# Kernel optimization log

Hardware: AMD Instinct MI355X
Metric: run time of the kernel (lower is better)

## Reference

```python
import jax, jax.numpy as jnp
import numpy as np

B = 2048
F = 267          # frame_size
L = 32           # latent_size
H = 256          # hidden_size (hard-coded in module)
E = 8            # num_experts
G = 64           # gate hidden size (hard-coded)
IN0 = L + F      # decoder layer0 input (latent + frame*cond_frames)
IN1 = L + H      # decoder inter input
OUT = F          # num_future_predictions * frame_size


def _lin_init(key, out_dim, in_dim):
    # kaiming-uniform-like scale
    bound = float(np.sqrt(1.0 / in_dim))
    return jax.random.uniform(key, (out_dim, in_dim), jnp.float32, -bound, bound)


def setup_inputs() -> dict:
    key = jax.random.key(0)
    ks = jax.random.split(key, 24)
    d = {}
    d["x"] = jax.random.normal(ks[0], (B, F), jnp.float32)
    d["c"] = jax.random.normal(ks[1], (B, F), jnp.float32)
    # encoder
    d["fc1_w"] = _lin_init(ks[2], H, 2 * F); d["fc1_b"] = jnp.zeros((H,), jnp.float32)
    d["fc2_w"] = _lin_init(ks[3], H, F + H); d["fc2_b"] = jnp.zeros((H,), jnp.float32)
    d["mu_w"] = _lin_init(ks[4], L, F + H);  d["mu_b"] = jnp.zeros((L,), jnp.float32)
    d["lv_w"] = _lin_init(ks[5], L, F + H);  d["lv_b"] = jnp.zeros((L,), jnp.float32)
    # gate
    d["g0_w"] = _lin_init(ks[6], G, IN0); d["g0_b"] = jnp.zeros((G,), jnp.float32)
    d["g1_w"] = _lin_init(ks[7], G, G);   d["g1_b"] = jnp.zeros((G,), jnp.float32)
    d["g2_w"] = _lin_init(ks[8], E, G);   d["g2_b"] = jnp.zeros((E,), jnp.float32)
    # expert weights [E, in, out], biases [E, out], bias filled 0.01 as in module
    d["w0"] = jax.random.uniform(ks[9], (E, IN0, H), jnp.float32, -1, 1) * np.sqrt(1.0 / IN0)
    d["b0"] = jnp.full((E, H), 0.01, jnp.float32)
    d["w1"] = jax.random.uniform(ks[10], (E, IN1, H), jnp.float32, -1, 1) * np.sqrt(1.0 / IN1)
    d["b1"] = jnp.full((E, H), 0.01, jnp.float32)
    d["w2"] = jax.random.uniform(ks[11], (E, IN1, OUT), jnp.float32, -1, 1) * np.sqrt(1.0 / IN1)
    d["b2"] = jnp.full((E, OUT), 0.01, jnp.float32)
    return d


def reference(x, c, fc1_w, fc1_b, fc2_w, fc2_b, mu_w, mu_b, lv_w, lv_b,
              g0_w, g0_b, g1_w, g1_b, g2_w, g2_b, w0, b0, w1, b1, w2, b2):
    elu = jax.nn.elu
    # ---- encoder ----
    h1 = elu(jnp.concatenate([x, c], axis=1) @ fc1_w.T + fc1_b)
    h2 = elu(jnp.concatenate([x, h1], axis=1) @ fc2_w.T + fc2_b)
    s = jnp.concatenate([x, h2], axis=1)
    mu = s @ mu_w.T + mu_b
    logvar = s @ lv_w.T + lv_b
    eps = jax.random.normal(jax.random.key(42), mu.shape, mu.dtype)
    z = mu + eps * jnp.exp(0.5 * logvar)
    # ---- mixed decoder ----
    g = elu(jnp.concatenate([z, c], axis=1) @ g0_w.T + g0_b)
    g = elu(g @ g1_w.T + g1_b)
    coeff = jax.nn.softmax(g @ g2_w.T + g2_b, axis=1)  # [B, E]
    layer_out = c
    for (W, bvec, act) in ((w0, b0, True), (w1, b1, True), (w2, b2, False)):
        inp = jnp.concatenate([z, layer_out], axis=1)          # [B, in]
        # per-expert GEMM then coefficient mixing (same math as per-sample
        # mixed-weight bmm: coeff @ flat_weight then baddbmm)
        out = jnp.einsum('be,bi,eio->bo', coeff, inp, W, optimize=True)
        out = out + coeff @ bvec                               # mixed bias
        layer_out = elu(out) if act else out
    return (layer_out, mu, logvar)
```

## Files before the change

### kernel.cpp

```cpp
#include <hip/hip_runtime.h>
#include <math.h>
#include <stdint.h>

#define DI __device__ __forceinline__

typedef __attribute__((ext_vector_type(8))) short bf16x8;
typedef __attribute__((ext_vector_type(4))) float f32x4;
typedef __attribute__((ext_vector_type(4))) int i32x4;

DI float elu_f(float v) { return v > 0.f ? v : expm1f(v); }

DI unsigned short f2bf(float f) {
  uint32_t u = __float_as_uint(f);
  return (unsigned short)((u + 0x7FFFu + ((u >> 16) & 1u)) >> 16);
}

DI void threefry2x32(uint32_t k0, uint32_t k1, uint32_t& x0, uint32_t& x1) {
  uint32_t ks0 = k0, ks1 = k1, ks2 = k0 ^ k1 ^ 0x1BD11BDAu;
  x0 += ks0; x1 += ks1;
#define TFR(r) { x0 += x1; x1 = (x1 << r) | (x1 >> (32 - r)); x1 ^= x0; }
  TFR(13) TFR(15) TFR(26) TFR(6)   x0 += ks1; x1 += ks2 + 1u;
  TFR(17) TFR(29) TFR(16) TFR(24)  x0 += ks2; x1 += ks0 + 2u;
  TFR(13) TFR(15) TFR(26) TFR(6)   x0 += ks0; x1 += ks1 + 3u;
  TFR(17) TFR(29) TFR(16) TFR(24)  x0 += ks1; x1 += ks2 + 4u;
  TFR(13) TFR(15) TFR(26) TFR(6)   x0 += ks2; x1 += ks0 + 5u;
#undef TFR
}

DI float erfinv_f(float x) {
  float w = -logf((1.0f - x) * (1.0f + x));
  float p;
  if (w < 5.0f) {
    w -= 2.5f;
    p = 2.81022636e-08f;
    p = fmaf(p, w, 3.43273939e-07f);
    p = fmaf(p, w, -3.5233877e-06f);
    p = fmaf(p, w, -4.39150654e-06f);
    p = fmaf(p, w, 0.00021858087f);
    p = fmaf(p, w, -0.00125372503f);
    p = fmaf(p, w, -0.00417768164f);
    p = fmaf(p, w, 0.246640727f);
    p = fmaf(p, w, 1.50140941f);
  } else {
    w = sqrtf(w) - 3.0f;
    p = -0.000200214257f;
    p = fmaf(p, w, 0.000100950558f);
    p = fmaf(p, w, 0.00134934322f);
    p = fmaf(p, w, -0.00367342844f);
    p = fmaf(p, w, 0.00573950773f);
    p = fmaf(p, w, -0.0076224613f);
    p = fmaf(p, w, 0.00943887047f);
    p = fmaf(p, w, 1.00167406f);
    p = fmaf(p, w, 2.83297682f);
  }
  return p * x;
}

struct MegaArgs {
  const float *x, *c;
  const float *fc1w, *fc1b, *fc2w, *fc2b, *muw, *mub, *lvw, *lvb;
  const float *g0w, *g0b, *g1w, *g1b, *g2w, *g2b;
  const float *w0, *b0, *w1, *b1, *w2, *b2;
  unsigned short *Ax, *Axh, *Axh2, *A0, *A1, *A2;
  unsigned short *fc1t, *fc2t, *mlvt, *g0t, *g1t, *w0b, *w1b, *w2b;
  float *cf, *outY, *outMu, *outLv;
};

template <int KT, int NE, int D, bool ELU, bool OUTF32>
__global__ __launch_bounds__(128, 2)
void pipe32(const unsigned short* __restrict__ A,
            const unsigned short* __restrict__ Wt, int N,
            const float* __restrict__ bias,
            const float* __restrict__ cfp,
            unsigned short* __restrict__ Cb, int ldcb, int cb_off,
            float* __restrict__ Cf) {
  constexpr int Kp = KT * 32, TT = NE * KT;
  __shared__ float bias_s[NE * 32];
  __shared__ float cfs[(NE > 1) ? 256 : 1];
  const int tid = threadIdx.x, lane = tid & 63, wv = tid >> 6;
  const int q = lane >> 4, l16 = lane & 15;
  const int m0 = blockIdx.x * 32;
  const int n0 = blockIdx.y * 32 + wv * 16;
  const int gc = n0 + l16;
  const int wrow = (gc < N) ? gc : (N - 1);
  const unsigned short* wlane = Wt + (size_t)wrow * Kp + q * 8;

  bf16x8 ring[D];
#pragma unroll
  for (int g = 0; g < D; g++) {
    if (g < TT) {
      int e = g / KT, c = g % KT;
      ring[g] = *(const bf16x8*)(wlane + (size_t)e * N * Kp + c * 32);
    }
  }
  bf16x8 areg[2][KT];
#pragma unroll
  for (int t = 0; t < 2; t++) {
    const unsigned short* alane = A + (size_t)(m0 + t * 16 + l16) * Kp + q * 8;
#pragma unroll
    for (int c = 0; c < KT; c++) areg[t][c] = *(const bf16x8*)(alane + c * 32);
  }

  if (NE == 1) {
    if (tid < 32) {
      int col = blockIdx.y * 32 + tid;
      bias_s[tid] = (col < N) ? bias[col] : 0.f;
    }
  } else {
    for (int idx = tid; idx < NE * 32; idx += 128) {
      int e = idx >> 5, col = blockIdx.y * 32 + (idx & 31);
      bias_s[idx] = (col < N) ? bias[(size_t)e * N + col] : 0.f;
    }
    for (int idx = tid; idx < 256; idx += 128)
      cfs[idx] = cfp[(size_t)(m0 + (idx >> 3)) * 8 + (idx & 7)];
  }
  __syncthreads();

  f32x4 acc[2] = {{0.f, 0.f, 0.f, 0.f}, {0.f, 0.f, 0.f, 0.f}};
  f32x4 accF[2] = {{0.f, 0.f, 0.f, 0.f}, {0.f, 0.f, 0.f, 0.f}};
#pragma unroll
  for (int g = 0; g < TT; g++) {
    const int e = g / KT, c = g % KT;
    bf16x8 bv = ring[g % D];
    acc[0] = __builtin_amdgcn_mfma_f32_16x16x32_bf16(areg[0][c], bv, acc[0], 0, 0, 0);
    acc[1] = __builtin_amdgcn_mfma_f32_16x16x32_bf16(areg[1][c], bv, acc[1], 0, 0, 0);
    if (g + D < TT) {
      int e2 = (g + D) / KT, c2 = (g + D) % KT;
      ring[g % D] = *(const bf16x8*)(wlane + (size_t)e2 * N * Kp + c2 * 32);
    }
    if (NE > 1 && c == KT - 1) {
      float bv2 = bias_s[e * 32 + wv * 16 + l16];
#pragma unroll
      for (int t = 0; t < 2; t++)
#pragma unroll
        for (int r = 0; r < 4; r++) {
          float ce = cfs[(t * 16 + q * 4 + r) * 8 + e];
          accF[t][r] += ce * (acc[t][r] + bv2);
          acc[t][r] = 0.f;
        }
    }
  }

  if (gc < N) {
#pragma unroll
    for (int t = 0; t < 2; t++)
#pragma unroll
      for (int r = 0; r < 4; r++) {
        int row = m0 + t * 16 + q * 4 + r;
        float v = (NE > 1) ? accF[t][r] : (acc[t][r] + bias_s[wv * 16 + l16]);
        if (ELU) v = elu_f(v);
        if (OUTF32) Cf[(size_t)row * 267 + gc] = v;
        else Cb[(size_t)row * ldcb + cb_off + gc] = f2bf(v);
      }
  }
}

__global__ __launch_bounds__(256) void k_prep(MegaArgs a) {
  __shared__ __align__(16) unsigned short T[64][72];
  const int bb = blockIdx.x, tid = threadIdx.x;
  if (bb < 512) {
    for (int rr = 0; rr < 4; rr++) {
      int b = bb * 4 + rr;
      const float* xr = a.x + (size_t)b * 267;
      const float* cr = a.c + (size_t)b * 267;
      unsigned short* axr = a.Ax + (size_t)b * 544;
      for (int k = tid; k < 544; k += 256) {
        float v = (k < 267) ? xr[k] : ((k < 534) ? cr[k - 267] : 0.f);
        axr[k] = f2bf(v);
      }
      unsigned short* ahr = a.Axh + (size_t)b * 544;
      unsigned short* ah2 = a.Axh2 + (size_t)b * 544;
      for (int k = tid; k < 267; k += 256) { unsigned short v = f2bf(xr[k]); ahr[k] = v; ah2[k] = v; }
      for (int k = 523 + tid; k < 544; k += 256) { ahr[k] = 0; ah2[k] = 0; }
      unsigned short* a0r = a.A0 + (size_t)b * 320;
      for (int k = tid; k < 288; k += 256)
        a0r[32 + k] = (k < 267) ? f2bf(cr[k]) : (unsigned short)0;
    }
  } else if (bb < 1152) {
    int r = bb - 512;
    const float* src; unsigned short* dst; int Ks, Kp2;
    if (r < 256)      { src = a.fc1w + (size_t)r * 534; dst = a.fc1t + (size_t)r * 544; Ks = 534; Kp2 = 544; }
    else if (r < 512) { int n = r - 256; src = a.fc2w + (size_t)n * 523; dst = a.fc2t + (size_t)n * 544; Ks = 523; Kp2 = 544; }
    else if (r < 576) { int n = r - 512; src = (n < 32) ? (a.muw + (size_t)n * 523) : (a.lvw + (size_t)(n - 32) * 523);
                        dst = a.mlvt + (size_t)n * 544; Ks = 523; Kp2 = 544; }
    else              { int n = r - 576; src = a.g0w + (size_t)n * 299; dst = a.g0t + (size_t)n * 320; Ks = 299; Kp2 = 320; }
    for (int k = tid; k < Kp2; k += 256) dst[k] = (k < Ks) ? f2bf(src[k]) : (unsigned short)0;
  } else if (bb == 1152) {
    for (int k = tid; k < 4096; k += 256) a.g1t[k] = f2bf(a.g1w[k]);
  } else {
    int t = bb - 1153;
    const float* W; unsigned short* D; int K, N2, Kp2, ldW, e, kt, nt;
    if (t < 160)      { e = t / 20;  int lt = t % 20;  kt = lt / 4; nt = lt % 4; W = a.w0; D = a.w0b; K = 299; N2 = 256; Kp2 = 320; ldW = 256; }
    else if (t < 320) { int u = t - 160; e = u / 20; int lt = u % 20; kt = lt / 4; nt = lt % 4; W = a.w1; D = a.w1b; K = 288; N2 = 256; Kp2 = 288; ldW = 256; }
    else              { int u = t - 320; e = u / 25; int lt = u % 25; kt = lt / 5; nt = lt % 5; W = a.w2; D = a.w2b; K = 288; N2 = 267; Kp2 = 288; ldW = 267; }
    const int k0 = kt * 64, n0 = nt * 64;
    const float* We = W + (size_t)e * K * ldW;
    const int jj = tid & 63, ii0 = tid >> 6;
#pragma unroll
    for (int p = 0; p < 16; p++) {
      int i = ii0 + p * 4;
      int gk = k0 + i, gn = n0 + jj;
      float v = (gk < K && gn < N2) ? We[(size_t)gk * ldW + gn] : 0.f;
      T[jj][i] = f2bf(v);
    }
    __syncthreads();
    int j = tid >> 2, chb = tid & 3;
    int gn = n0 + j;
    if (gn < N2) {
      unsigned short* drow = D + ((size_t)e * N2 + gn) * Kp2 + k0;
#pragma unroll
      for (int s = 0; s < 2; s++) {
        int ch = chb + s * 4;
        if (k0 + ch * 8 < Kp2) {
          i32x4 v = *(i32x4*)(&T[j][ch * 8]);
          *(i32x4*)(drow + ch * 8) = v;
        }
      }
    }
  }
}

__global__ __launch_bounds__(256, 2) void k_mulv_gate(MegaArgs a) {
  __shared__ float mlvS[16 * 65];
  __shared__ __align__(16) unsigned short A0p[16 * 328];
  __shared__ __align__(16) unsigned short gaB[16 * 72];
  __shared__ __align__(16) unsigned short g1B[64 * 72];
  __shared__ float g2wT[64 * 8];
  __shared__ float gB[16 * 65];
  __shared__ float lg[16 * 8];
  const int tid = threadIdx.x, lane = tid & 63, wid = tid >> 6;
  const int q = lane >> 4, l16 = lane & 15;
  const int m0 = blockIdx.x * 16;
  const int cl = wid * 16 + l16;

  const unsigned short* alane = a.Axh2 + (size_t)(m0 + l16) * 544 + q * 8;
  const unsigned short* wlA = a.mlvt + (size_t)cl * 544 + q * 8;
  bf16x8 ring[8];
#pragma unroll
  for (int g = 0; g < 8; g++) ring[g] = *(const bf16x8*)(wlA + g * 32);
  bf16x8 areg[17];
#pragma unroll
  for (int c = 0; c < 17; c++) areg[c] = *(const bf16x8*)(alane + c * 32);
  f32x4 acc = {0.f, 0.f, 0.f, 0.f};
#pragma unroll
  for (int g = 0; g < 17; g++) {
    acc = __builtin_amdgcn_mfma_f32_16x16x32_bf16(areg[g], ring[g % 8], acc, 0, 0, 0);
    if (g + 8 < 17) ring[g % 8] = *(const bf16x8*)(wlA + (g + 8) * 32);
  }
#pragma unroll
  for (int r = 0; r < 4; r++) mlvS[(q * 4 + r) * 65 + cl] = acc[r];
  for (int idx = tid; idx < 576; idx += 256) {
    int row = idx / 36, ch = 4 + idx % 36;
    *(i32x4*)(A0p + row * 328 + ch * 8) =
        *(const i32x4*)(a.A0 + (size_t)(m0 + row) * 320 + ch * 8);
  }
  if (tid < 16) { i32x4 z4 = {0, 0, 0, 0}; *(i32x4*)(A0p + tid * 328 + 320) = z4; }
  for (int idx = tid; idx < 512; idx += 256) {
    int row = idx >> 3, ch = idx & 7;
    *(i32x4*)(g1B + row * 72 + ch * 8) = *(const i32x4*)(a.g1t + (size_t)row * 64 + ch * 8);
  }
  for (int idx = tid; idx < 512; idx += 256)
    g2wT[(idx & 63) * 8 + (idx >> 6)] = a.g2w[idx];
  __syncthreads();

  {
    const int m = tid >> 4, j0 = (tid & 15) * 2, R = m0 + m;
#pragma unroll
    for (int jj = 0; jj < 2; jj++) {
      int j = j0 + jj;
      float mu = mlvS[m * 65 + j] + a.mub[j];
      float lvv = mlvS[m * 65 + j + 32] + a.lvb[j];
      uint32_t x0 = 0u, x1 = (uint32_t)(R * 32 + j);
      threefry2x32(0u, 42u, x0, x1);
      uint32_t bits = x0 ^ x1;
      float f = __uint_as_float((bits >> 9) | 0x3F800000u) - 1.0f;
      const float lo = -0.99999994039535522461f;
      float u = fmaf(f, 2.0f, lo);
      u = fmaxf(u, lo);
      float eps = 1.41421356237f * erfinv_f(u);
      float z = fmaf(eps, expf(0.5f * lvv), mu);
      a.outMu[(size_t)R * 32 + j] = mu;
      a.outLv[(size_t)R * 32 + j] = lvv;
      unsigned short zb = f2bf(z);
      A0p[m * 328 + j] = zb;
      a.A0[(size_t)R * 320 + j] = zb;
      a.A1[(size_t)R * 288 + j] = zb;
      a.A2[(size_t)R * 288 + j] = zb;
    }
  }
  __syncthreads();

  const unsigned short* wlC = a.g0t + (size_t)cl * 320 + q * 8;
  bf16x8 ring2[8];
#pragma unroll
  for (int g = 0; g < 8; g++) ring2[g] = *(const bf16x8*)(wlC + g * 32);
  f32x4 accC = {0.f, 0.f, 0.f, 0.f};
#pragma unroll
  for (int g = 0; g < 10; g++) {
    bf16x8 av = *(const bf16x8*)(A0p + l16 * 328 + g * 32 + q * 8);
    accC = __builtin_amdgcn_mfma_f32_16x16x32_bf16(av, ring2[g % 8], accC, 0, 0, 0);
    if (g + 8 < 10) ring2[g % 8] = *(const bf16x8*)(wlC + (g + 8) * 32);
  }
  {
    float bc = a.g0b[cl];
#pragma unroll
    for (int r = 0; r < 4; r++)
      gaB[(q * 4 + r) * 72 + cl] = f2bf(elu_f(accC[r] + bc));
  }
  __syncthreads();

  f32x4 accD = {0.f, 0.f, 0.f, 0.f};
#pragma unroll
  for (int tau = 0; tau < 2; tau++) {
    bf16x8 av = *(const bf16x8*)(gaB + l16 * 72 + tau * 32 + q * 8);
    bf16x8 bv = *(const bf16x8*)(g1B + cl * 72 + tau * 32 + q * 8);
    accD = __builtin_amdgcn_mfma_f32_16x16x32_bf16(av, bv, accD, 0, 0, 0);
  }
  {
    float bc = a.g1b[cl];
#pragma unroll
    for (int r = 0; r < 4; r++)
      gB[(q * 4 + r) * 65 + cl] = elu_f(accD[r] + bc);
  }
  __syncthreads();

  if (tid < 128) {
    int r = tid >> 3, e = tid & 7;
    float d = a.g2b[e];
#pragma unroll 8
    for (int k = 0; k < 64; k++) d = fmaf(gB[r * 65 + k], g2wT[k * 8 + e], d);
    lg[r * 8 + e] = d;
  }
  __syncthreads();
  if (tid < 16) {
    float mx = lg[tid * 8];
#pragma unroll
    for (int e2 = 1; e2 < 8; e2++) mx = fmaxf(mx, lg[tid * 8 + e2]);
    float s = 0.f, ex[8];
#pragma unroll
    for (int e2 = 0; e2 < 8; e2++) { ex[e2] = expf(lg[tid * 8 + e2] - mx); s += ex[e2]; }
    float inv = 1.f / s;
#pragma unroll
    for (int e2 = 0; e2 < 8; e2++) a.cf[(size_t)(m0 + tid) * 8 + e2] = ex[e2] * inv;
  }
}

extern "C" void kernel_launch(void* const* d_in, const int* in_sizes, int n_in,
                              void* d_out, int out_size, void* d_ws, size_t ws_size,
                              hipStream_t stream) {
  (void)in_sizes; (void)n_in; (void)out_size; (void)ws_size;
  float* out = (float*)d_out;
  float* ws = (float*)d_ws;

  MegaArgs a;
  a.x    = (const float*)d_in[0];
  a.c    = (const float*)d_in[1];
  a.fc1w = (const float*)d_in[2];  a.fc1b = (const float*)d_in[3];
  a.fc2w = (const float*)d_in[4];  a.fc2b = (const float*)d_in[5];
  a.muw  = (const float*)d_in[6];  a.mub  = (const float*)d_in[7];
  a.lvw  = (const float*)d_in[8];  a.lvb  = (const float*)d_in[9];
  a.g0w  = (const float*)d_in[10]; a.g0b  = (const float*)d_in[11];
  a.g1w  = (const float*)d_in[12]; a.g1b  = (const float*)d_in[13];
  a.g2w  = (const float*)d_in[14]; a.g2b  = (const float*)d_in[15];
  a.w0   = (const float*)d_in[16]; a.b0   = (const float*)d_in[17];
  a.w1   = (const float*)d_in[18]; a.b1   = (const float*)d_in[19];
  a.w2   = (const float*)d_in[20]; a.b2   = (const float*)d_in[21];

  a.outY  = out;
  a.outMu = out + 2048 * 267;
  a.outLv = a.outMu + 2048 * 32;

  a.Ax   = (unsigned short*)(ws);
  a.Axh  = (unsigned short*)(ws + 557056);
  a.Axh2 = (unsigned short*)(ws + 1114112);
  a.A0   = (unsigned short*)(ws + 1671168);
  a.A1   = (unsigned short*)(ws + 1998848);
  a.A2   = (unsigned short*)(ws + 2293760);
  a.fc1t = (unsigned short*)(ws + 2588672);
  a.fc2t = (unsigned short*)(ws + 2658304);
  a.mlvt = (unsigned short*)(ws + 2727936);
  a.g0t  = (unsigned short*)(ws + 2745344);
  a.g1t  = (unsigned short*)(ws + 2755584);
  a.w0b  = (unsigned short*)(ws + 2757632);
  a.w1b  = (unsigned short*)(ws + 3085312);
  a.w2b  = (unsigned short*)(ws + 3380224);
  a.cf   = ws + 3687808;

  dim3 blkP(256), blkG(128);
  k_prep<<<1673, blkP, 0, stream>>>(a);
  pipe32<17, 1, 12, true, false><<<dim3(64, 8), blkG, 0, stream>>>(
      a.Ax, a.fc1t, 256, a.fc1b, nullptr, a.Axh, 544, 267, nullptr);
  pipe32<17, 1, 12, true, false><<<dim3(64, 8), blkG, 0, stream>>>(
      a.Axh, a.fc2t, 256, a.fc2b, nullptr, a.Axh2, 544, 267, nullptr);
  k_mulv_gate<<<128, blkP, 0, stream>>>(a);
  pipe32<10, 8, 12, true, false><<<dim3(64, 8), blkG, 0, stream>>>(
      a.A0, a.w0b, 256, a.b0, a.cf, a.A1, 288, 32, nullptr);
  pipe32<9, 8, 12, true, false><<<dim3(64, 8), blkG, 0, stream>>>(
      a.A1, a.w1b, 256, a.b1, a.cf, a.A2, 288, 32, nullptr);
  pipe32<9, 8, 12, false, true><<<dim3(64, 9), blkG, 0, stream>>>(
      a.A2, a.w2b, 267, a.b2, a.cf, nullptr, 0, 0, a.outY);
}
```

Baseline: 175.8 us.

## Fuse fc2 into mu/logvar-gate kernel and overlap weight prep with encoder

Reworks the launch plan from seven kernels to six. fc1 weight conversion stays in the first prep kernel. The fc1 GEMM now runs in the same launch as the remaining weight conversions and part of the expert weight transposes. The fc2 GEMM moves into the mu/logvar/gate kernel, with the fc2 output kept in shared memory, which removes the Axh2 buffer and a launch boundary; the rest of the transposes fill spare blocks of that kernel. This aims to cut launch overhead and a global round-trip and to hide weight preprocessing behind compute. In exchange, fc2 now runs on only 128 blocks with 4 serial column tiles per wave, which may reduce parallelism.

```diff
diff --git a/kernel.cpp b/kernel.cpp
--- a/kernel.cpp
+++ b/kernel.cpp
@@ -7,6 +7,8 @@
 typedef __attribute__((ext_vector_type(8))) short bf16x8;
 typedef __attribute__((ext_vector_type(4))) float f32x4;
 typedef __attribute__((ext_vector_type(4))) int i32x4;
+
+#define MFMA16(av, bv, acc) __builtin_amdgcn_mfma_f32_16x16x32_bf16(av, bv, acc, 0, 0, 0)
 
 DI float elu_f(float v) { return v > 0.f ? v : expm1f(v); }
 
@@ -61,7 +63,7 @@
   const float *fc1w, *fc1b, *fc2w, *fc2b, *muw, *mub, *lvw, *lvb;
   const float *g0w, *g0b, *g1w, *g1b, *g2w, *g2b;
   const float *w0, *b0, *w1, *b1, *w2, *b2;
-  unsigned short *Ax, *Axh, *Axh2, *A0, *A1, *A2;
+  unsigned short *Ax, *Axh, *A0, *A1, *A2;
   unsigned short *fc1t, *fc2t, *mlvt, *g0t, *g1t, *w0b, *w1b, *w2b;
   float *cf, *outY, *outMu, *outLv;
 };
@@ -122,8 +124,8 @@
   for (int g = 0; g < TT; g++) {
     const int e = g / KT, c = g % KT;
     bf16x8 bv = ring[g % D];
-    acc[0] = __builtin_amdgcn_mfma_f32_16x16x32_bf16(areg[0][c], bv, acc[0], 0, 0, 0);
-    acc[1] = __builtin_amdgcn_mfma_f32_16x16x32_bf16(areg[1][c], bv, acc[1], 0, 0, 0);
+    acc[0] = MFMA16(areg[0][c], bv, acc[0]);
+    acc[1] = MFMA16(areg[1][c], bv, acc[1]);
     if (g + D < TT) {
       int e2 = (g + D) / KT, c2 = (g + D) % KT;
       ring[g % D] = *(const bf16x8*)(wlane + (size_t)e2 * N * Kp + c2 * 32);
@@ -155,8 +157,84 @@
   }
 }
 
-__global__ __launch_bounds__(256) void k_prep(MegaArgs a) {
-  __shared__ __align__(16) unsigned short T[64][72];
+DI void transpose_params(int t, const MegaArgs& a, const float*& W,
+                         unsigned short*& D, int& K, int& N2, int& Kp2,
+                         int& ldW, int& e, int& kt, int& nt) {
+  if (t < 160)      { e = t / 20;  int lt = t % 20;  kt = lt / 4; nt = lt % 4; W = a.w0; D = a.w0b; K = 299; N2 = 256; Kp2 = 320; ldW = 256; }
+  else if (t < 320) { int u = t - 160; e = u / 20; int lt = u % 20; kt = lt / 4; nt = lt % 4; W = a.w1; D = a.w1b; K = 288; N2 = 256; Kp2 = 288; ldW = 256; }
+  else              { int u = t - 320; e = u / 25; int lt = u % 25; kt = lt / 5; nt = lt % 5; W = a.w2; D = a.w2b; K = 288; N2 = 267; Kp2 = 288; ldW = 267; }
+}
+
+DI void transpose128(unsigned short (*T)[72], int t, const MegaArgs& a) {
+  const int tid = threadIdx.x;
+  const float* W; unsigned short* D; int K, N2, Kp2, ldW, e, kt, nt;
+  transpose_params(t, a, W, D, K, N2, Kp2, ldW, e, kt, nt);
+  const int k0 = kt * 64, n0 = nt * 64;
+  const float* We = W + (size_t)e * K * ldW;
+  const int jj = tid & 63, ii0 = tid >> 6;
+#pragma unroll
+  for (int p = 0; p < 32; p++) {
+    int i = ii0 + p * 2;
+    int gk = k0 + i, gn = n0 + jj;
+    float v = (gk < K && gn < N2) ? We[(size_t)gk * ldW + gn] : 0.f;
+    T[jj][i] = f2bf(v);
+  }
+  __syncthreads();
+  const int j0 = tid >> 2, chb = tid & 3;
+#pragma unroll
+  for (int jh = 0; jh < 2; jh++) {
+    int j = j0 + jh * 32;
+    int gn = n0 + j;
+    if (gn < N2) {
+      unsigned short* drow = D + ((size_t)e * N2 + gn) * Kp2 + k0;
+#pragma unroll
+      for (int s = 0; s < 2; s++) {
+        int ch = chb + s * 4;
+        if (k0 + ch * 8 < Kp2) {
+          i32x4 v = *(i32x4*)(&T[j][ch * 8]);
+          *(i32x4*)(drow + ch * 8) = v;
+        }
+      }
+    }
+  }
+}
+
+DI void transpose256(unsigned short (*T)[72], int t, const MegaArgs& a) {
+  const int tid = threadIdx.x;
+  const float* W; unsigned short* D; int K, N2, Kp2, ldW, e, kt, nt;
+  transpose_params(t, a, W, D, K, N2, Kp2, ldW, e, kt, nt);
+  const int k0 = kt * 64, n0 = nt * 64;
+  const float* We = W + (size_t)e * K * ldW;
+  const int jj = tid & 63, ii0 = tid >> 6;
+#pragma unroll
+  for (int p = 0; p < 16; p++) {
+    int i = ii0 + p * 4;
+    int gk = k0 + i, gn = n0 + jj;
+    float v = (gk < K && gn < N2) ? We[(size_t)gk * ldW + gn] : 0.f;
+    T[jj][i] = f2bf(v);
+  }
+  __syncthreads();
+  int j = tid >> 2, chb = tid & 3;
+  int gn = n0 + j;
+  if (gn < N2) {
+    unsigned short* drow = D + ((size_t)e * N2 + gn) * Kp2 + k0;
+#pragma unroll
+    for (int s = 0; s < 2; s++) {
+      int ch = chb + s * 4;
+      if (k0 + ch * 8 < Kp2) {
+        i32x4 v = *(i32x4*)(&T[j][ch * 8]);
+        *(i32x4*)(drow + ch * 8) = v;
+      }
+    }
+  }
+}
+
+DI void conv128(const float* src, unsigned short* dst, int Ks, int Kp2) {
+  for (int k = threadIdx.x; k < Kp2; k += 128)
+    dst[k] = (k < Ks) ? f2bf(src[k]) : (unsigned short)0;
+}
+
+__global__ __launch_bounds__(256) void k_prep0(MegaArgs a) {
   const int bb = blockIdx.x, tid = threadIdx.x;
   if (bb < 512) {
     for (int rr = 0; rr < 4; rr++) {
@@ -169,58 +247,80 @@
         axr[k] = f2bf(v);
       }
       unsigned short* ahr = a.Axh + (size_t)b * 544;
-      unsigned short* ah2 = a.Axh2 + (size_t)b * 544;
-      for (int k = tid; k < 267; k += 256) { unsigned short v = f2bf(xr[k]); ahr[k] = v; ah2[k] = v; }
-      for (int k = 523 + tid; k < 544; k += 256) { ahr[k] = 0; ah2[k] = 0; }
+      for (int k = tid; k < 267; k += 256) ahr[k] = f2bf(xr[k]);
+      for (int k = 523 + tid; k < 544; k += 256) ahr[k] = 0;
       unsigned short* a0r = a.A0 + (size_t)b * 320;
       for (int k = tid; k < 288; k += 256)
         a0r[32 + k] = (k < 267) ? f2bf(cr[k]) : (unsigned short)0;
     }
-  } else if (bb < 1152) {
+  } else {
     int r = bb - 512;
-    const float* src; unsigned short* dst; int Ks, Kp2;
-    if (r < 256)      { src = a.fc1w + (size_t)r * 534; dst = a.fc1t + (size_t)r * 544; Ks = 534; Kp2 = 544; }
-    else if (r < 512) { int n = r - 256; src = a.fc2w + (size_t)n * 523; dst = a.fc2t + (size_t)n * 544; Ks = 523; Kp2 = 544; }
-    else if (r < 576) { int n = r - 512; src = (n < 32) ? (a.muw + (size_t)n * 523) : (a.lvw + (size_t)(n - 32) * 523);
-                        dst = a.mlvt + (size_t)n * 544; Ks = 523; Kp2 = 544; }
-    else              { int n = r - 576; src = a.g0w + (size_t)n * 299; dst = a.g0t + (size_t)n * 320; Ks = 299; Kp2 = 320; }
-    for (int k = tid; k < Kp2; k += 256) dst[k] = (k < Ks) ? f2bf(src[k]) : (unsigned short)0;
-  } else if (bb == 1152) {
-    for (int k = tid; k < 4096; k += 256) a.g1t[k] = f2bf(a.g1w[k]);
+    const float* src = a.fc1w + (size_t)r * 534;
+    unsigned short* dst = a.fc1t + (size_t)r * 544;
+    for (int k = tid; k < 544; k += 256)
+      dst[k] = (k < 534) ? f2bf(src[k]) : (unsigned short)0;
+  }
+}
+
+__global__ __launch_bounds__(128, 2) void k_fc1mix(MegaArgs a) {
+  __shared__ float bias_s[32];
+  __shared__ __align__(16) unsigned short T[64][72];
+  const int bid = blockIdx.x, tid = threadIdx.x;
+  if (bid < 512) {
+    const int lane = tid & 63, wv = tid >> 6;
+    const int q = lane >> 4, l16 = lane & 15;
+    const int bx = bid & 63, by = bid >> 6;
+    const int m0 = bx * 32;
+    const int gc = by * 32 + wv * 16 + l16;
+    const unsigned short* wlane = a.fc1t + (size_t)gc * 544 + q * 8;
+
+    bf16x8 ring[12];
+#pragma unroll
+    for (int g = 0; g < 12; g++)
+      ring[g] = *(const bf16x8*)(wlane + g * 32);
+    bf16x8 areg[2][17];
+#pragma unroll
+    for (int t = 0; t < 2; t++) {
+      const unsigned short* alane = a.Ax + (size_t)(m0 + t * 16 + l16) * 544 + q * 8;
+#pragma unroll
+      for (int c = 0; c < 17; c++) areg[t][c] = *(const bf16x8*)(alane + c * 32);
+    }
+    if (tid < 32) bias_s[tid] = a.fc1b[by * 32 + tid];
+    __syncthreads();
+
+    f32x4 acc[2] = {{0.f, 0.f, 0.f, 0.f}, {0.f, 0.f, 0.f, 0.f}};
+#pragma unroll
+    for (int g = 0; g < 17; g++) {
+      bf16x8 bv = ring[g % 12];
+      acc[0] = MFMA16(areg[0][g], bv, acc[0]);
+      acc[1] = MFMA16(areg[1][g], bv, acc[1]);
+      if (g + 12 < 17)
+        ring[g % 12] = *(const bf16x8*)(wlane + (g + 12) * 32);
+    }
+    float bc = bias_s[wv * 16 + l16];
+#pragma unroll
+    for (int t = 0; t < 2; t++)
+#pragma unroll
+      for (int r = 0; r < 4; r++) {
+        int row = m0 + t * 16 + q * 4 + r;
+        a.Axh[(size_t)row * 544 + 267 + gc] = f2bf(elu_f(acc[t][r] + bc));
+      }
+  } else if (bid < 897) {
+    int c = bid - 512;
+    if (c < 256)      conv128(a.fc2w + (size_t)c * 523, a.fc2t + (size_t)c * 544, 523, 544);
+    else if (c < 320) { int n = c - 256;
+                        conv128((n < 32) ? (a.muw + (size_t)n * 523) : (a.lvw + (size_t)(n - 32) * 523),
+                                a.mlvt + (size_t)n * 544, 523, 544); }
+    else if (c < 384) { int n = c - 320;
+                        conv128(a.g0w + (size_t)n * 299, a.g0t + (size_t)n * 320, 299, 320); }
+    else              conv128(a.g1w, a.g1t, 4096, 4096);
   } else {
-    int t = bb - 1153;
-    const float* W; unsigned short* D; int K, N2, Kp2, ldW, e, kt, nt;
-    if (t < 160)      { e = t / 20;  int lt = t % 20;  kt = lt / 4; nt = lt % 4; W = a.w0; D = a.w0b; K = 299; N2 = 256; Kp2 = 320; ldW = 256; }
-    else if (t < 320) { int u = t - 160; e = u / 20; int lt = u % 20; kt = lt / 4; nt = lt % 4; W = a.w1; D = a.w1b; K = 288; N2 = 256; Kp2 = 288; ldW = 256; }
-    else              { int u = t - 320; e = u / 25; int lt = u % 25; kt = lt / 5; nt = lt % 5; W = a.w2; D = a.w2b; K = 288; N2 = 267; Kp2 = 288; ldW = 267; }
-    const int k0 = kt * 64, n0 = nt * 64;
-    const float* We = W + (size_t)e * K * ldW;
-    const int jj = tid & 63, ii0 = tid >> 6;
-#pragma unroll
-    for (int p = 0; p < 16; p++) {
-      int i = ii0 + p * 4;
-      int gk = k0 + i, gn = n0 + jj;
-      float v = (gk < K && gn < N2) ? We[(size_t)gk * ldW + gn] : 0.f;
-      T[jj][i] = f2bf(v);
-    }
-    __syncthreads();
-    int j = tid >> 2, chb = tid & 3;
-    int gn = n0 + j;
-    if (gn < N2) {
-      unsigned short* drow = D + ((size_t)e * N2 + gn) * Kp2 + k0;
-#pragma unroll
-      for (int s = 0; s < 2; s++) {
-        int ch = chb + s * 4;
-        if (k0 + ch * 8 < Kp2) {
-          i32x4 v = *(i32x4*)(&T[j][ch * 8]);
-          *(i32x4*)(drow + ch * 8) = v;
-        }
-      }
-    }
-  }
-}
-
-__global__ __launch_bounds__(256, 2) void k_mulv_gate(MegaArgs a) {
+    transpose128(T, bid - 897, a);
+  }
+}
+
+__global__ __launch_bounds__(256) void k_enc(MegaArgs a) {
+  __shared__ __align__(16) unsigned short sA[16][552];
   __shared__ float mlvS[16 * 65];
   __shared__ __align__(16) unsigned short A0p[16 * 328];
   __shared__ __align__(16) unsigned short gaB[16 * 72];
@@ -228,27 +328,66 @@
   __shared__ float g2wT[64 * 8];
   __shared__ float gB[16 * 65];
   __shared__ float lg[16 * 8];
+  __shared__ __align__(16) unsigned short T[64][72];
+
+  const int bid = blockIdx.x;
+  if (bid >= 128) { transpose256(T, 160 + (bid - 128), a); return; }
+
   const int tid = threadIdx.x, lane = tid & 63, wid = tid >> 6;
   const int q = lane >> 4, l16 = lane & 15;
-  const int m0 = blockIdx.x * 16;
+  const int m0 = bid * 16;
+
+  for (int idx = tid; idx < 16 * 68; idx += 256) {
+    int row = idx / 68, ch = idx % 68;
+    *(i32x4*)(&sA[row][ch * 8]) =
+        *(const i32x4*)(a.Axh + (size_t)(m0 + row) * 544 + ch * 8);
+  }
+  bf16x8 areg[17];
+  {
+    const unsigned short* alane = a.Axh + (size_t)(m0 + l16) * 544 + q * 8;
+#pragma unroll
+    for (int c = 0; c < 17; c++) areg[c] = *(const bf16x8*)(alane + c * 32);
+  }
+  for (int idx = tid; idx < 512; idx += 256)
+    g2wT[(idx & 63) * 8 + (idx >> 6)] = a.g2w[idx];
+  __syncthreads();
+
+#pragma unroll
+  for (int i = 0; i < 4; i++) {
+    const int col = (wid * 4 + i) * 16 + l16;
+    const unsigned short* wl = a.fc2t + (size_t)col * 544 + q * 8;
+    bf16x8 ring[8];
+#pragma unroll
+    for (int g = 0; g < 8; g++) ring[g] = *(const bf16x8*)(wl + g * 32);
+    f32x4 acc = {0.f, 0.f, 0.f, 0.f};
+#pragma unroll
+    for (int g = 0; g < 17; g++) {
+      acc = MFMA16(areg[g], ring[g % 8], acc);
+      if (g + 8 < 17) ring[g % 8] = *(const bf16x8*)(wl + (g + 8) * 32);
+    }
+    float bc = a.fc2b[col];
+#pragma unroll
+    for (int r = 0; r < 4; r++)
+      sA[q * 4 + r][267 + col] = f2bf(elu_f(acc[r] + bc));
+  }
+  __syncthreads();
+
   const int cl = wid * 16 + l16;
-
-  const unsigned short* alane = a.Axh2 + (size_t)(m0 + l16) * 544 + q * 8;
-  const unsigned short* wlA = a.mlvt + (size_t)cl * 544 + q * 8;
-  bf16x8 ring[8];
-#pragma unroll
-  for (int g = 0; g < 8; g++) ring[g] = *(const bf16x8*)(wlA + g * 32);
-  bf16x8 areg[17];
-#pragma unroll
-  for (int c = 0; c < 17; c++) areg[c] = *(const bf16x8*)(alane + c * 32);
-  f32x4 acc = {0.f, 0.f, 0.f, 0.f};
-#pragma unroll
-  for (int g = 0; g < 17; g++) {
-    acc = __builtin_amdgcn_mfma_f32_16x16x32_bf16(areg[g], ring[g % 8], acc, 0, 0, 0);
-    if (g + 8 < 17) ring[g % 8] = *(const bf16x8*)(wlA + (g + 8) * 32);
-  }
-#pragma unroll
-  for (int r = 0; r < 4; r++) mlvS[(q * 4 + r) * 65 + cl] = acc[r];
+  {
+    const unsigned short* wlA = a.mlvt + (size_t)cl * 544 + q * 8;
+    bf16x8 ring[8];
+#pragma unroll
+    for (int g = 0; g < 8; g++) ring[g] = *(const bf16x8*)(wlA + g * 32);
+    f32x4 acc = {0.f, 0.f, 0.f, 0.f};
+#pragma unroll
+    for (int g = 0; g < 17; g++) {
+      bf16x8 av = *(const bf16x8*)(&sA[l16][g * 32 + q * 8]);
+      acc = MFMA16(av, ring[g % 8], acc);
+      if (g + 8 < 17) ring[g % 8] = *(const bf16x8*)(wlA + (g + 8) * 32);
+    }
+#pragma unroll
+    for (int r = 0; r < 4; r++) mlvS[(q * 4 + r) * 65 + cl] = acc[r];
+  }
   for (int idx = tid; idx < 576; idx += 256) {
     int row = idx / 36, ch = 4 + idx % 36;
     *(i32x4*)(A0p + row * 328 + ch * 8) =
@@ -259,8 +398,6 @@
     int row = idx >> 3, ch = idx & 7;
     *(i32x4*)(g1B + row * 72 + ch * 8) = *(const i32x4*)(a.g1t + (size_t)row * 64 + ch * 8);
   }
-  for (int idx = tid; idx < 512; idx += 256)
-    g2wT[(idx & 63) * 8 + (idx >> 6)] = a.g2w[idx];
   __syncthreads();
 
   {
@@ -290,18 +427,18 @@
   }
   __syncthreads();
 
-  const unsigned short* wlC = a.g0t + (size_t)cl * 320 + q * 8;
-  bf16x8 ring2[8];
-#pragma unroll
-  for (int g = 0; g < 8; g++) ring2[g] = *(const bf16x8*)(wlC + g * 32);
-  f32x4 accC = {0.f, 0.f, 0.f, 0.f};
-#pragma unroll
-  for (int g = 0; g < 10; g++) {
-    bf16x8 av = *(const bf16x8*)(A0p + l16 * 328 + g * 32 + q * 8);
-    accC = __builtin_amdgcn_mfma_f32_16x16x32_bf16(av, ring2[g % 8], accC, 0, 0, 0);
-    if (g + 8 < 10) ring2[g % 8] = *(const bf16x8*)(wlC + (g + 8) * 32);
-  }
   {
+    const unsigned short* wlC = a.g0t + (size_t)cl * 320 + q * 8;
+    bf16x8 ring2[8];
+#pragma unroll
+    for (int g = 0; g < 8; g++) ring2[g] = *(const bf16x8*)(wlC + g * 32);
+    f32x4 accC = {0.f, 0.f, 0.f, 0.f};
+#pragma unroll
+    for (int g = 0; g < 10; g++) {
+      bf16x8 av = *(const bf16x8*)(A0p + l16 * 328 + g * 32 + q * 8);
+      accC = MFMA16(av, ring2[g % 8], accC);
+      if (g + 8 < 10) ring2[g % 8] = *(const bf16x8*)(wlC + (g + 8) * 32);
+    }
     float bc = a.g0b[cl];
 #pragma unroll
     for (int r = 0; r < 4; r++)
@@ -309,14 +446,14 @@
   }
   __syncthreads();
 
-  f32x4 accD = {0.f, 0.f, 0.f, 0.f};
-#pragma unroll
-  for (int tau = 0; tau < 2; tau++) {
-    bf16x8 av = *(const bf16x8*)(gaB + l16 * 72 + tau * 32 + q * 8);
-    bf16x8 bv = *(const bf16x8*)(g1B + cl * 72 + tau * 32 + q * 8);
-    accD = __builtin_amdgcn_mfma_f32_16x16x32_bf16(av, bv, accD, 0, 0, 0);
-  }
   {
+    f32x4 accD = {0.f, 0.f, 0.f, 0.f};
+#pragma unroll
+    for (int tau = 0; tau < 2; tau++) {
+      bf16x8 av = *(const bf16x8*)(gaB + l16 * 72 + tau * 32 + q * 8);
+      bf16x8 bv = *(const bf16x8*)(g1B + cl * 72 + tau * 32 + q * 8);
+      accD = MFMA16(av, bv, accD);
+    }
     float bc = a.g1b[cl];
 #pragma unroll
     for (int r = 0; r < 4; r++)
@@ -372,7 +509,6 @@
 
   a.Ax   = (unsigned short*)(ws);
   a.Axh  = (unsigned short*)(ws + 557056);
-  a.Axh2 = (unsigned short*)(ws + 1114112);
   a.A0   = (unsigned short*)(ws + 1671168);
   a.A1   = (unsigned short*)(ws + 1998848);
   a.A2   = (unsigned short*)(ws + 2293760);
@@ -386,17 +522,13 @@
   a.w2b  = (unsigned short*)(ws + 3380224);
   a.cf   = ws + 3687808;
 
-  dim3 blkP(256), blkG(128);
-  k_prep<<<1673, blkP, 0, stream>>>(a);
-  pipe32<17, 1, 12, true, false><<<dim3(64, 8), blkG, 0, stream>>>(
-      a.Ax, a.fc1t, 256, a.fc1b, nullptr, a.Axh, 544, 267, nullptr);
-  pipe32<17, 1, 12, true, false><<<dim3(64, 8), blkG, 0, stream>>>(
-      a.Axh, a.fc2t, 256, a.fc2b, nullptr, a.Axh2, 544, 267, nullptr);
-  k_mulv_gate<<<128, blkP, 0, stream>>>(a);
-  pipe32<10, 8, 12, true, false><<<dim3(64, 8), blkG, 0, stream>>>(
+  k_prep0<<<768, 256, 0, stream>>>(a);
+  k_fc1mix<<<1057, 128, 0, stream>>>(a);
+  k_enc<<<488, 256, 0, stream>>>(a);
+  pipe32<10, 8, 12, true, false><<<dim3(64, 8), 128, 0, stream>>>(
       a.A0, a.w0b, 256, a.b0, a.cf, a.A1, 288, 32, nullptr);
-  pipe32<9, 8, 12, true, false><<<dim3(64, 8), blkG, 0, stream>>>(
+  pipe32<9, 8, 12, true, false><<<dim3(64, 8), 128, 0, stream>>>(
       a.A1, a.w1b, 256, a.b1, a.cf, a.A2, 288, 32, nullptr);
-  pipe32<9, 8, 12, false, true><<<dim3(64, 9), blkG, 0, stream>>>(
+  pipe32<9, 8, 12, false, true><<<dim3(64, 9), 128, 0, stream>>>(
       a.A2, a.w2b, 267, a.b2, a.cf, nullptr, 0, 0, a.outY);
 }
```

New measurement: 189.5 us. 1.08x slower.
